# Kernel tuning notes

Hardware: AMD Instinct MI355X
Metric: run time of the kernel (lower is better)

Reference implementation:

```python
import jax, jax.numpy as jnp
import numpy as np

B, S, D_MODEL = 2, 2048, 2048
H, DS, DG, DV = 16, 64, 64, 128
ROPE_BASE = 10000.0
NEG_INF = -1e9


def _rope(x, base=ROPE_BASE):
    # x: [B, S, H, D] -> rotate-half RoPE over positions 0..S-1
    d = x.shape[-1]
    half = d // 2
    inv_freq = 1.0 / (base ** (jnp.arange(half, dtype=jnp.float32) / half))
    ang = jnp.arange(x.shape[1], dtype=jnp.float32)[:, None] * inv_freq  # [S, half]
    cos = jnp.cos(ang)[None, :, None, :]
    sin = jnp.sin(ang)[None, :, None, :]
    x1, x2 = x[..., :half], x[..., half:]
    return jnp.concatenate([x1 * cos - x2 * sin, x1 * sin + x2 * cos], axis=-1)


def setup_inputs() -> dict:
    key = jax.random.key(0)
    ks = jax.random.split(key, 8)
    s = lambda fan_in: 1.0 / np.sqrt(fan_in)
    return {
        "x": jax.random.normal(ks[0], (B, S, D_MODEL), dtype=jnp.float32),
        "wq_sem": jax.random.normal(ks[1], (D_MODEL, H * DS), dtype=jnp.float32) * s(D_MODEL),
        "wk_sem": jax.random.normal(ks[2], (D_MODEL, H * DS), dtype=jnp.float32) * s(D_MODEL),
        "wq_geo": jax.random.normal(ks[3], (D_MODEL, H * DG), dtype=jnp.float32) * s(D_MODEL),
        "wk_geo": jax.random.normal(ks[4], (D_MODEL, H * DG), dtype=jnp.float32) * s(D_MODEL),
        "wv": jax.random.normal(ks[5], (D_MODEL, H * DV), dtype=jnp.float32) * s(D_MODEL),
        "wo": jax.random.normal(ks[6], (H * DV, D_MODEL), dtype=jnp.float32) * s(H * DV),
        "gate_logit": jax.random.normal(ks[7], (H,), dtype=jnp.float32),
    }


def reference(x, wq_sem, wk_sem, wq_geo, wk_geo, wv, wo, gate_logit):
    b, sl, _ = x.shape
    # Projections -> [B, S, H, d]
    qs = (x @ wq_sem).reshape(b, sl, H, DS)
    ksem = (x @ wk_sem).reshape(b, sl, H, DS)
    qg = _rope((x @ wq_geo).reshape(b, sl, H, DG))
    kg = _rope((x @ wk_geo).reshape(b, sl, H, DG))
    v = (x @ wv).reshape(b, sl, H, DV)

    sem_scale = 1.0 / np.sqrt(DS)
    geo_scale = 1.0 / np.sqrt(DG)
    sem_scores = jnp.einsum("bqhd,bkhd->bhqk", qs, ksem) * sem_scale
    geo_scores = jnp.einsum("bqhd,bkhd->bhqk", qg, kg) * geo_scale

    # Learned per-head gate mixing semantic vs geometric paths
    g = jax.nn.sigmoid(gate_logit)[None, :, None, None]
    scores = g * sem_scores + (1.0 - g) * geo_scores

    causal = jnp.tril(jnp.ones((sl, sl), dtype=bool))
    scores = jnp.where(causal[None, None], scores, NEG_INF)
    attn = jax.nn.softmax(scores, axis=-1)

    out = jnp.einsum("bhqk,bkhd->bqhd", attn, v).reshape(b, sl, H * DV)
    return out @ wo
```

## Files before the change

### kernel.cpp

```cpp
#include <hip/hip_runtime.h>
#include <hip/hip_bf16.h>

typedef unsigned short u16;
typedef __attribute__((ext_vector_type(4))) float floatx4;
typedef __attribute__((ext_vector_type(8))) __bf16 bf16x8;

__device__ __forceinline__ u16 f2bf(float f) {
  unsigned int x = __builtin_bit_cast(unsigned int, f);
  unsigned int r = (x + 0x7fffu + ((x >> 16) & 1u)) >> 16;
  return (u16)r;
}
__device__ __forceinline__ float bf2f(u16 u) {
  unsigned int x = ((unsigned int)u) << 16;
  return __builtin_bit_cast(float, x);
}
__device__ __forceinline__ floatx4 mfma16(bf16x8 a, bf16x8 b, floatx4 c) {
  return __builtin_amdgcn_mfma_f32_16x16x32_bf16(a, b, c, 0, 0, 0);
}
__device__ __forceinline__ void gload16(const u16* g, u16* l) {
  __builtin_amdgcn_global_load_lds(
      (const __attribute__((address_space(1))) unsigned int*)g,
      (__attribute__((address_space(3))) unsigned int*)l, 16, 0, 0);
}
#define SCHEDB() __builtin_amdgcn_sched_barrier(0)
#define SBAR() __builtin_amdgcn_s_barrier()

#define BB 2
#define SS 2048
#define DM 2048
#define HH 16
#define PCOLS 6144

__global__ void convert_bf16_k(const float* __restrict__ src, u16* __restrict__ dst, size_t n) {
  size_t i = ((size_t)blockIdx.x * blockDim.x + threadIdx.x) * 4;
  if (i + 3 >= n) { for (size_t j = i; j < n; ++j) dst[j] = f2bf(src[j]); return; }
  float4 v = *(const float4*)&src[i];
  ushort4 o; o.x = f2bf(v.x); o.y = f2bf(v.y); o.z = f2bf(v.z); o.w = f2bf(v.w);
  *(ushort4*)&dst[i] = o;
}

__global__ void transpose_all_k(const float* w0, const float* w1, const float* w2,
                                const float* w3, const float* w4, const float* w5,
                                u16* __restrict__ WcatT, u16* __restrict__ WoT) {
  __shared__ float tile[32][33];
  const int z = blockIdx.z;
  const float* src; u16* dst; int cols;
  if (z == 0)      { src = w0; dst = WcatT;                        cols = 1024; }
  else if (z == 1) { src = w1; dst = WcatT + (size_t)1024 * 2048;  cols = 1024; }
  else if (z == 2) { src = w2; dst = WcatT + (size_t)2048 * 2048;  cols = 1024; }
  else if (z == 3) { src = w3; dst = WcatT + (size_t)3072 * 2048;  cols = 1024; }
  else if (z == 4) { src = w4; dst = WcatT + (size_t)4096 * 2048;  cols = 2048; }
  else             { src = w5; dst = WoT;                          cols = 2048; }
  int c0 = blockIdx.x * 32;
  if (c0 >= cols) return;
  int r0 = blockIdx.y * 32;
  int tx = threadIdx.x, ty = threadIdx.y;
#pragma unroll
  for (int i = 0; i < 4; ++i)
    tile[ty + i * 8][tx] = src[(size_t)(r0 + ty + i * 8) * cols + c0 + tx];
  __syncthreads();
#pragma unroll
  for (int i = 0; i < 4; ++i)
    dst[(size_t)(c0 + ty + i * 8) * 2048 + r0 + tx] = f2bf(tile[tx][ty + i * 8]);
}

__global__ void vtrans_k(const u16* __restrict__ P, u16* __restrict__ VtG) {
  __shared__ u16 t[32][33];
  int b = blockIdx.z;
  int c0 = blockIdx.x * 32;
  int s0 = blockIdx.y * 32;
  int tx = threadIdx.x, ty = threadIdx.y;
#pragma unroll
  for (int i = 0; i < 4; ++i)
    t[ty + i * 8][tx] = P[((size_t)b * SS + s0 + ty + i * 8) * PCOLS + 4096 + c0 + tx];
  __syncthreads();
#pragma unroll
  for (int i = 0; i < 4; ++i)
    VtG[((size_t)b * 2048 + c0 + ty + i * 8) * SS + s0 + tx] = t[tx][ty + i * 8];
}

__global__ void rope_table_k(float* __restrict__ cosT, float* __restrict__ sinT) {
  int idx = blockIdx.x * 256 + threadIdx.x;
  int s = idx >> 5, d = idx & 31;
  double inv = pow(10000.0, -(double)d / 32.0);
  double ang = (double)s * inv;
  cosT[idx] = (float)cos(ang);
  sinT[idx] = (float)sin(ang);
}

__global__ void rope_apply_k(u16* __restrict__ P, const float* __restrict__ cosT,
                             const float* __restrict__ sinT) {
  int idx = blockIdx.x * 256 + threadIdx.x;
  int d = idx & 31, h = (idx >> 5) & 15, reg = (idx >> 9) & 1, row = idx >> 10;
  int s = row & (SS - 1);
  size_t base = (size_t)row * PCOLS + (reg ? 3072 : 2048) + h * 64 + d;
  float x1 = bf2f(P[base]), x2 = bf2f(P[base + 32]);
  float c = cosT[s * 32 + d], sn = sinT[s * 32 + d];
  P[base] = f2bf(x1 * c - x2 * sn);
  P[base + 32] = f2bf(x1 * sn + x2 * c);
}

template <bool OUTF32>
__global__ __launch_bounds__(512, 2)
void gemm8_k(const u16* __restrict__ A, const u16* __restrict__ Bt,
             void* __restrict__ Cout, int M, int N, int K) {
  __shared__ alignas(16) u16 lds[49152];
  const int tid = threadIdx.x;
  const int wid = tid >> 6, lane = tid & 63;
  const int lr = lane & 15, lg = lane >> 4;
  const int wr = wid >> 2, wc = wid & 3;
  const int m0 = blockIdx.y * 128, n0 = blockIdx.x * 256;
  const int NT = K >> 6;
  const int NT4 = NT * 4;

  const int gA = ((lg ^ ((lr >> 1) & 3)) * 8);
  const int aoffL = lr * 32 + gA;

  const int srow = tid >> 2;
  const int sgl = (((tid & 3) ^ ((tid >> 3) & 3)) * 8);
  const u16* Asrc = A + (size_t)(m0 + srow) * K + sgl;
  const u16* Bsrc0 = Bt + (size_t)(n0 + srow) * K + sgl;
  const u16* Bsrc1 = Bsrc0 + (size_t)128 * K;
  const int wbase = wid * 512;

  floatx4 acc[4][4];
#pragma unroll
  for (int m = 0; m < 4; ++m)
#pragma unroll
    for (int n = 0; n < 4; ++n) acc[m][n] = (floatx4){0.f, 0.f, 0.f, 0.f};

  auto stgA = [&](int tile, int kh) {
    gload16(Asrc + tile * 64 + kh * 32,
            lds + ((tile & 1) * 2 + kh) * 4096 + wbase);
  };
  auto stgB = [&](int tile, int kh) {
    u16* d = lds + 16384 + ((tile & 1) * 2 + kh) * 8192 + wbase;
    const u16* s0 = Bsrc0 + tile * 64 + kh * 32;
    const u16* s1 = Bsrc1 + tile * 64 + kh * 32;
    gload16(s0, d);
    gload16(s1, d + 4096);
  };
  auto stage_slab = [&](int s) {
    if (s >= NT4) return;
    int tile = s >> 2, kind = s & 3;
    if (kind == 0) stgA(tile, 0);
    else if (kind == 1) stgB(tile, 0);
    else if (kind == 2) stgA(tile, 1);
    else stgB(tile, 1);
  };

  for (int s = 0; s < 7; ++s) stage_slab(s);
  asm volatile("s_waitcnt vmcnt(4)" ::: "memory");
  SCHEDB(); SBAR(); SCHEDB();

  bf16x8 af[4], bfv[2];

#pragma unroll 1
  for (int it = 0; it < (NT >> 1); ++it) {
    const int t = it * 2;
    const int sb = t * 4 + 6;
    const bool more = (t + 2 < NT);

#define PH(BUF, KK, NH, SL, DOVM)                                              \
    {                                                                          \
      const u16* Ab = lds + ((BUF) * 2 + (KK)) * 4096;                         \
      const u16* Bb = lds + 16384 + ((BUF) * 2 + (KK)) * 8192;                 \
      if ((NH) == 0) {                                                         \
        _Pragma("unroll") for (int m = 0; m < 4; ++m)                          \
          af[m] = *(const bf16x8*)&Ab[(wr * 64 + m * 16) * 32 + aoffL];        \
      }                                                                        \
      _Pragma("unroll") for (int j = 0; j < 2; ++j)                            \
        bfv[j] = *(const bf16x8*)&Bb[(wc * 64 + ((NH) * 2 + j) * 16) * 32 + aoffL]; \
      stage_slab(sb + (SL));                                                   \
      SCHEDB(); SBAR(); SCHEDB();                                              \
      __builtin_amdgcn_s_setprio(1);                                           \
      _Pragma("unroll") for (int m = 0; m < 4; ++m)                            \
        _Pragma("unroll") for (int j = 0; j < 2; ++j)                          \
          acc[m][(NH) * 2 + j] = mfma16(af[m], bfv[j], acc[m][(NH) * 2 + j]);  \
      __builtin_amdgcn_s_setprio(0);                                           \
      if (DOVM) {                                                              \
        if (more) asm volatile("s_waitcnt vmcnt(4)" ::: "memory");             \
        else      asm volatile("s_waitcnt vmcnt(0)" ::: "memory");             \
      }                                                                        \
      SCHEDB(); SBAR(); SCHEDB();                                              \
    }

    PH(0, 0, 0, 1, 0)
    PH(0, 0, 1, 2, 0)
    PH(0, 1, 0, 3, 0)
    PH(0, 1, 1, 4, 1)
    PH(1, 0, 0, 5, 0)
    PH(1, 0, 1, 6, 0)
    PH(1, 1, 0, 7, 0)
    PH(1, 1, 1, 8, 1)
#undef PH
  }

#pragma unroll
  for (int m = 0; m < 4; ++m) {
    int row0 = m0 + wr * 64 + m * 16 + lg * 4;
#pragma unroll
    for (int n = 0; n < 4; ++n) {
      int col = n0 + wc * 64 + n * 16 + lr;
#pragma unroll
      for (int r = 0; r < 4; ++r) {
        size_t off = (size_t)(row0 + r) * N + col;
        if (OUTF32) ((float*)Cout)[off] = acc[m][n][r];
        else        ((u16*)Cout)[off] = f2bf(acc[m][n][r]);
      }
    }
  }
}

__device__ __forceinline__ bf16x8 load_scaled(const u16* p, float s) {
  uint4 raw = *(const uint4*)p;
  const u16* ru = (const u16*)&raw;
  bf16x8 out;
#pragma unroll
  for (int j = 0; j < 8; ++j) out[j] = (__bf16)(bf2f(ru[j]) * s);
  return out;
}

__global__ __launch_bounds__(256, 3)
void attn_k(const u16* __restrict__ P, const u16* __restrict__ VtG,
            const float* __restrict__ gate, u16* __restrict__ AttO) {
  const int pairi = blockIdx.x >> 4;
  const int h = blockIdx.x & 15;
  const int b = blockIdx.y;
  const int tid = threadIdx.x, wid = tid >> 6, lane = tid & 63;
  const int lr = lane & 15, lg = lane >> 4;
  const size_t rowb = (size_t)b * SS;

  const float g = 1.f / (1.f + __expf(-gate[h]));
  const float ssc = g * 0.125f;
  const float gsc = (1.f - g) * 0.125f;

  __shared__ alignas(16) u16 Ks[64 * 64];
  __shared__ alignas(16) u16 Kg[64 * 64];
  __shared__ alignas(16) u16 Vt[128 * 64];
  __shared__ alignas(16) u16 Pw[4][16 * 64];

  const int strow = tid >> 3;
  const int stg = ((tid & 7) ^ (strow & 7)) * 8;
  const int swz = lr & 7;

  for (int half = 0; half < 2; ++half) {
    const int qb = half ? (31 - pairi) : pairi;
    const int q0 = qb * 64;

    const u16* qbase = P + (rowb + q0 + wid * 16 + lr) * PCOLS + h * 64;
    bf16x8 qs[2], qg[2];
#pragma unroll
    for (int kk = 0; kk < 2; ++kk) {
      qs[kk] = load_scaled(qbase + kk * 32 + lg * 8, ssc);
      qg[kk] = load_scaled(qbase + 2048 + kk * 32 + lg * 8, gsc);
    }

    float m_r = -1e30f, l_r = 0.f;
    floatx4 o[8];
#pragma unroll
    for (int n = 0; n < 8; ++n) o[n] = (floatx4){0.f, 0.f, 0.f, 0.f};

    const int nkv = q0 + 64;
    for (int kv0 = 0; kv0 < nkv; kv0 += 64) {
      __syncthreads();
      {
        const u16* ks = P + (rowb + kv0 + strow) * PCOLS + 1024 + h * 64 + stg;
        const u16* gs = P + (rowb + kv0 + strow) * PCOLS + 3072 + h * 64 + stg;
        gload16(ks, Ks + wid * 512);
        gload16(gs, Kg + wid * 512);
        gload16(ks + (size_t)32 * PCOLS, Ks + 2048 + wid * 512);
        gload16(gs + (size_t)32 * PCOLS, Kg + 2048 + wid * 512);
      }
      {
        const u16* vs = VtG + ((size_t)b * 2048 + h * 128 + strow) * SS + kv0 + stg;
#pragma unroll
        for (int c = 0; c < 4; ++c)
          gload16(vs + (size_t)(c * 32) * SS, Vt + c * 2048 + wid * 512);
      }
      __syncthreads();

      floatx4 sc[4];
#pragma unroll
      for (int s = 0; s < 4; ++s) sc[s] = (floatx4){0.f, 0.f, 0.f, 0.f};
#pragma unroll
      for (int kk = 0; kk < 2; ++kk) {
#pragma unroll
        for (int s = 0; s < 4; ++s) {
          bf16x8 kf = *(const bf16x8*)&Ks[(s * 16 + lr) * 64 + ((kk * 4 + lg) ^ swz) * 8];
          bf16x8 gf = *(const bf16x8*)&Kg[(s * 16 + lr) * 64 + ((kk * 4 + lg) ^ swz) * 8];
          sc[s] = mfma16(kf, qs[kk], sc[s]);
          sc[s] = mfma16(gf, qg[kk], sc[s]);
        }
      }

      const int qrow = q0 + wid * 16 + lr;
      const bool needmask = (kv0 + 63 > q0 + wid * 16);
      float vv[4][4];
      float vmax = -1e30f;
#pragma unroll
      for (int s = 0; s < 4; ++s)
#pragma unroll
        for (int r = 0; r < 4; ++r) {
          float val = sc[s][r];
          if (needmask) val = (kv0 + s * 16 + lg * 4 + r <= qrow) ? val : -1e30f;
          vv[s][r] = val;
          vmax = fmaxf(vmax, val);
        }
      vmax = fmaxf(vmax, __shfl_xor(vmax, 16));
      vmax = fmaxf(vmax, __shfl_xor(vmax, 32));
      float mnew = fmaxf(m_r, vmax);
      float corr = __expf(m_r - mnew);
      float psum = 0.f;
#pragma unroll
      for (int s = 0; s < 4; ++s)
#pragma unroll
        for (int r = 0; r < 4; ++r) {
          vv[s][r] = __expf(vv[s][r] - mnew);
          psum += vv[s][r];
        }
      psum += __shfl_xor(psum, 16);
      psum += __shfl_xor(psum, 32);
      l_r = l_r * corr + psum;
      m_r = mnew;

#pragma unroll
      for (int s = 0; s < 4; ++s)
#pragma unroll
        for (int t = 0; t < 2; ++t) {
          unsigned int w;
          asm("v_cvt_pk_bf16_f32 %0, %1, %2" : "=v"(w) : "v"(vv[s][2 * t]), "v"(vv[s][2 * t + 1]));
          int u16off = lr * 64 + ((s * 2 + (lg >> 1)) ^ swz) * 8 + (lg & 1) * 4 + t * 2;
          *(unsigned int*)&Pw[wid][u16off] = w;
        }

      float crr[4];
#pragma unroll
      for (int r = 0; r < 4; ++r) crr[r] = __shfl(corr, lg * 4 + r);
#pragma unroll
      for (int n = 0; n < 8; ++n)
#pragma unroll
        for (int r = 0; r < 4; ++r) o[n][r] *= crr[r];

      asm volatile("s_waitcnt lgkmcnt(0)" ::: "memory");
      SCHEDB();
      bf16x8 pa0 = *(const bf16x8*)&Pw[wid][lr * 64 + (lg ^ swz) * 8];
      bf16x8 pa1 = *(const bf16x8*)&Pw[wid][lr * 64 + ((4 + lg) ^ swz) * 8];
#pragma unroll
      for (int n = 0; n < 8; ++n) {
        bf16x8 vb0 = *(const bf16x8*)&Vt[(n * 16 + lr) * 64 + (lg ^ swz) * 8];
        bf16x8 vb1 = *(const bf16x8*)&Vt[(n * 16 + lr) * 64 + ((4 + lg) ^ swz) * 8];
        o[n] = mfma16(pa0, vb0, o[n]);
        o[n] = mfma16(pa1, vb1, o[n]);
      }
    }

    float linv = 1.f / l_r;
    float lnv[4];
#pragma unroll
    for (int r = 0; r < 4; ++r) lnv[r] = __shfl(linv, lg * 4 + r);
#pragma unroll
    for (int n = 0; n < 8; ++n)
#pragma unroll
      for (int r = 0; r < 4; ++r) {
        float val = o[n][r] * lnv[r];
        AttO[(rowb + q0 + wid * 16 + lg * 4 + r) * (size_t)(HH * 128) + h * 128 + n * 16 + lr] =
            f2bf(val);
      }
  }
}

extern "C" void kernel_launch(void* const* d_in, const int* in_sizes, int n_in,
                              void* d_out, int out_size, void* d_ws, size_t ws_size,
                              hipStream_t stream) {
  const float* x       = (const float*)d_in[0];
  const float* wq_sem  = (const float*)d_in[1];
  const float* wk_sem  = (const float*)d_in[2];
  const float* wq_geo  = (const float*)d_in[3];
  const float* wk_geo  = (const float*)d_in[4];
  const float* wv      = (const float*)d_in[5];
  const float* wo      = (const float*)d_in[6];
  const float* gate    = (const float*)d_in[7];

  char* ws = (char*)d_ws;
  u16* Xbf   = (u16*)(ws);
  u16* WcatT = (u16*)(ws + 16777216);
  u16* WoT   = (u16*)(ws + 16777216 + 25165824);
  u16* P     = (u16*)(ws + 16777216 + 25165824 + 8388608);
  float* cosT = (float*)(ws + 16777216 + 25165824 + 8388608 + 50331648);
  float* sinT = cosT + 2048 * 32;
  u16* AttO = Xbf;
  u16* VtG  = WcatT;

  dim3 tb(32, 8);
  convert_bf16_k<<<8192, 256, 0, stream>>>(x, Xbf, (size_t)4096 * 2048);
  transpose_all_k<<<dim3(64, 64, 6), tb, 0, stream>>>(wq_sem, wk_sem, wq_geo, wk_geo,
                                                      wv, wo, WcatT, WoT);
  rope_table_k<<<256, 256, 0, stream>>>(cosT, sinT);

  gemm8_k<false><<<dim3(24, 32), 512, 0, stream>>>(Xbf, WcatT, P, 4096, 6144, 2048);
  rope_apply_k<<<16384, 256, 0, stream>>>(P, cosT, sinT);
  vtrans_k<<<dim3(64, 64, 2), tb, 0, stream>>>(P, VtG);
  attn_k<<<dim3(256, 2), 256, 0, stream>>>(P, VtG, gate, AttO);
  gemm8_k<true><<<dim3(8, 32), 512, 0, stream>>>(AttO, WoT, d_out, 4096, 2048, 2048);
}
```

Before: 272.2 us.

## Replace 8-wave GEMM with 4-wave kernel using larger per-wave tiles

The 512-thread GEMM (128x256 tile, 2x4 wave grid) is replaced by a 256-thread, one-block-per-SM kernel in which each wave computes all 128 rows against its own NFB*16 columns. The QKV projection now uses 128x384 tiles (512 blocks instead of 768) and the output projection uses 128x256 tiles. Larger per-wave register tiles raise MFMA work per LDS fragment load. The cost is more accumulator registers, fewer resident waves to hide latency, and changed vmcnt wait thresholds.

```diff
diff --git a/kernel.cpp b/kernel.cpp
--- a/kernel.cpp
+++ b/kernel.cpp
@@ -100,48 +100,46 @@
   P[base + 32] = f2bf(x1 * sn + x2 * c);
 }
 
-template <bool OUTF32>
-__global__ __launch_bounds__(512, 2)
-void gemm8_k(const u16* __restrict__ A, const u16* __restrict__ Bt,
+template <int NFB, bool OUTF32>
+__global__ __launch_bounds__(256, 1)
+void gemm4_k(const u16* __restrict__ A, const u16* __restrict__ Bt,
              void* __restrict__ Cout, int M, int N, int K) {
-  __shared__ alignas(16) u16 lds[49152];
+  constexpr int BH = NFB / 2;
+  __shared__ alignas(16) u16 lds[16384 + NFB * 8192];
   const int tid = threadIdx.x;
   const int wid = tid >> 6, lane = tid & 63;
   const int lr = lane & 15, lg = lane >> 4;
-  const int wr = wid >> 2, wc = wid & 3;
-  const int m0 = blockIdx.y * 128, n0 = blockIdx.x * 256;
+  const int m0 = blockIdx.y * 128, n0 = blockIdx.x * (NFB * 64);
   const int NT = K >> 6;
-  const int NT4 = NT * 4;
-
-  const int gA = ((lg ^ ((lr >> 1) & 3)) * 8);
-  const int aoffL = lr * 32 + gA;
-
-  const int srow = tid >> 2;
-  const int sgl = (((tid & 3) ^ ((tid >> 3) & 3)) * 8);
+  const int NSLAB = NT * 4;
+
+  const int aoff = lr * 32 + ((lg ^ ((lr >> 1) & 3)) * 8);
+
+  const int srow = wid * 16 + (lane >> 2);
+  const int sgl = (((lane & 3) ^ ((lane >> 3) & 3)) * 8);
   const u16* Asrc = A + (size_t)(m0 + srow) * K + sgl;
-  const u16* Bsrc0 = Bt + (size_t)(n0 + srow) * K + sgl;
-  const u16* Bsrc1 = Bsrc0 + (size_t)128 * K;
-  const int wbase = wid * 512;
-
-  floatx4 acc[4][4];
-#pragma unroll
-  for (int m = 0; m < 4; ++m)
-#pragma unroll
-    for (int n = 0; n < 4; ++n) acc[m][n] = (floatx4){0.f, 0.f, 0.f, 0.f};
+  const u16* Bsrc = Bt + (size_t)(n0 + srow) * K + sgl;
+
+  floatx4 acc[8][NFB];
+#pragma unroll
+  for (int m = 0; m < 8; ++m)
+#pragma unroll
+    for (int n = 0; n < NFB; ++n) acc[m][n] = (floatx4){0.f, 0.f, 0.f, 0.f};
 
   auto stgA = [&](int tile, int kh) {
-    gload16(Asrc + tile * 64 + kh * 32,
-            lds + ((tile & 1) * 2 + kh) * 4096 + wbase);
+    u16* d = lds + ((tile & 1) * 2 + kh) * 4096 + wid * 512;
+    const u16* s = Asrc + tile * 64 + kh * 32;
+#pragma unroll
+    for (int c = 0; c < 2; ++c) gload16(s + (size_t)(c * 64) * K, d + c * 2048);
   };
   auto stgB = [&](int tile, int kh) {
-    u16* d = lds + 16384 + ((tile & 1) * 2 + kh) * 8192 + wbase;
-    const u16* s0 = Bsrc0 + tile * 64 + kh * 32;
-    const u16* s1 = Bsrc1 + tile * 64 + kh * 32;
-    gload16(s0, d);
-    gload16(s1, d + 4096);
+    u16* d = lds + 16384 + ((tile & 1) * 2 + kh) * (NFB * 2048) + wid * 512;
+    const u16* s = Bsrc + tile * 64 + kh * 32;
+#pragma unroll
+    for (int c = 0; c < NFB; ++c) gload16(s + (size_t)(c * 64) * K, d + c * 2048);
   };
   auto stage_slab = [&](int s) {
-    if (s >= NT4) return;
+    if (s >= NSLAB) return;
     int tile = s >> 2, kind = s & 3;
     if (kind == 0) stgA(tile, 0);
     else if (kind == 1) stgB(tile, 0);
@@ -150,10 +148,11 @@
   };
 
   for (int s = 0; s < 7; ++s) stage_slab(s);
-  asm volatile("s_waitcnt vmcnt(4)" ::: "memory");
+  if constexpr (NFB == 6) asm volatile("s_waitcnt vmcnt(10)" ::: "memory");
+  else                    asm volatile("s_waitcnt vmcnt(8)" ::: "memory");
   SCHEDB(); SBAR(); SCHEDB();
 
-  bf16x8 af[4], bfv[2];
+  bf16x8 af[8], bfv[BH];
 
 #pragma unroll 1
   for (int it = 0; it < (NT >> 1); ++it) {
@@ -161,28 +160,32 @@
     const int sb = t * 4 + 6;
     const bool more = (t + 2 < NT);
 
-#define PH(BUF, KK, NH, SL, DOVM)                                              \
-    {                                                                          \
-      const u16* Ab = lds + ((BUF) * 2 + (KK)) * 4096;                         \
-      const u16* Bb = lds + 16384 + ((BUF) * 2 + (KK)) * 8192;                 \
-      if ((NH) == 0) {                                                         \
-        _Pragma("unroll") for (int m = 0; m < 4; ++m)                          \
-          af[m] = *(const bf16x8*)&Ab[(wr * 64 + m * 16) * 32 + aoffL];        \
-      }                                                                        \
-      _Pragma("unroll") for (int j = 0; j < 2; ++j)                            \
-        bfv[j] = *(const bf16x8*)&Bb[(wc * 64 + ((NH) * 2 + j) * 16) * 32 + aoffL]; \
-      stage_slab(sb + (SL));                                                   \
-      SCHEDB(); SBAR(); SCHEDB();                                              \
-      __builtin_amdgcn_s_setprio(1);                                           \
-      _Pragma("unroll") for (int m = 0; m < 4; ++m)                            \
-        _Pragma("unroll") for (int j = 0; j < 2; ++j)                          \
-          acc[m][(NH) * 2 + j] = mfma16(af[m], bfv[j], acc[m][(NH) * 2 + j]);  \
-      __builtin_amdgcn_s_setprio(0);                                           \
-      if (DOVM) {                                                              \
-        if (more) asm volatile("s_waitcnt vmcnt(4)" ::: "memory");             \
-        else      asm volatile("s_waitcnt vmcnt(0)" ::: "memory");             \
-      }                                                                        \
-      SCHEDB(); SBAR(); SCHEDB();                                              \
+#define PH(BUF, KK, NH, SL, DOVM)                                               \
+    {                                                                           \
+      const u16* Ab = lds + ((BUF) * 2 + (KK)) * 4096;                          \
+      const u16* Bb = lds + 16384 + ((BUF) * 2 + (KK)) * (NFB * 2048);          \
+      if ((NH) == 0) {                                                          \
+        _Pragma("unroll") for (int m = 0; m < 8; ++m)                           \
+          af[m] = *(const bf16x8*)&Ab[(m * 16) * 32 + aoff];                    \
+      }                                                                         \
+      _Pragma("unroll") for (int j = 0; j < BH; ++j)                            \
+        bfv[j] = *(const bf16x8*)&Bb[(wid * NFB * 16 + ((NH) * BH + j) * 16) * 32 + aoff]; \
+      stage_slab(sb + (SL));                                                    \
+      SCHEDB(); SBAR(); SCHEDB();                                               \
+      __builtin_amdgcn_s_setprio(1);                                            \
+      _Pragma("unroll") for (int m = 0; m < 8; ++m)                             \
+        _Pragma("unroll") for (int j = 0; j < BH; ++j)                          \
+          acc[m][(NH) * BH + j] = mfma16(af[m], bfv[j], acc[m][(NH) * BH + j]); \
+      __builtin_amdgcn_s_setprio(0);                                            \
+      if (DOVM) {                                                               \
+        if (more) {                                                             \
+          if constexpr (NFB == 6) asm volatile("s_waitcnt vmcnt(10)" ::: "memory"); \
+          else                    asm volatile("s_waitcnt vmcnt(8)" ::: "memory");  \
+        } else {                                                                \
+          asm volatile("s_waitcnt vmcnt(0)" ::: "memory");                      \
+        }                                                                       \
+      }                                                                         \
+      SCHEDB(); SBAR(); SCHEDB();                                               \
     }
 
     PH(0, 0, 0, 1, 0)
@@ -197,11 +200,11 @@
   }
 
 #pragma unroll
-  for (int m = 0; m < 4; ++m) {
-    int row0 = m0 + wr * 64 + m * 16 + lg * 4;
-#pragma unroll
-    for (int n = 0; n < 4; ++n) {
-      int col = n0 + wc * 64 + n * 16 + lr;
+  for (int m = 0; m < 8; ++m) {
+    int row0 = m0 + m * 16 + lg * 4;
+#pragma unroll
+    for (int n = 0; n < NFB; ++n) {
+      int col = n0 + wid * NFB * 16 + n * 16 + lr;
 #pragma unroll
       for (int r = 0; r < 4; ++r) {
         size_t off = (size_t)(row0 + r) * N + col;
@@ -398,9 +401,9 @@
                                                       wv, wo, WcatT, WoT);
   rope_table_k<<<256, 256, 0, stream>>>(cosT, sinT);
 
-  gemm8_k<false><<<dim3(24, 32), 512, 0, stream>>>(Xbf, WcatT, P, 4096, 6144, 2048);
+  gemm4_k<6, false><<<dim3(16, 32), 256, 0, stream>>>(Xbf, WcatT, P, 4096, 6144, 2048);
   rope_apply_k<<<16384, 256, 0, stream>>>(P, cosT, sinT);
   vtrans_k<<<dim3(64, 64, 2), tb, 0, stream>>>(P, VtG);
   attn_k<<<dim3(256, 2), 256, 0, stream>>>(P, VtG, gate, AttO);
-  gemm8_k<true><<<dim3(8, 32), 512, 0, stream>>>(AttO, WoT, d_out, 4096, 2048, 2048);
-}
+  gemm4_k<4, true><<<dim3(8, 32), 256, 0, stream>>>(AttO, WoT, d_out, 4096, 2048, 2048);
+}
```

After: 266.0 us. 1.02x faster.

## Restructure GEMM pipeline into coarser half-tile phases with XCD-aware block swizzle

Applied to the files above, without the earlier changes.

Rewrites the GEMM main loop from eight fine-grained phases, each issuing one A or B slab, into four phases. Each phase loads all 16 MFMA operand fragments and stages a combined A+B half-tile. It also remaps the block index with a modulo-8 swizzle so neighbouring tiles land on the same chiplet for L2 reuse, and lowers the occupancy hint to one block per CU. The aim is fewer barriers and better cache locality, at the cost of a deeper vmcnt wait window and possibly lower occupancy or register pressure changes.

```diff
diff --git a/kernel.cpp b/kernel.cpp
--- a/kernel.cpp
+++ b/kernel.cpp
@@ -101,27 +101,27 @@
 }
 
 template <bool OUTF32>
-__global__ __launch_bounds__(512, 2)
-void gemm8_k(const u16* __restrict__ A, const u16* __restrict__ Bt,
+__global__ __launch_bounds__(512, 1)
+void gemm2_k(const u16* __restrict__ A, const u16* __restrict__ Bt,
              void* __restrict__ Cout, int M, int N, int K) {
   __shared__ alignas(16) u16 lds[49152];
   const int tid = threadIdx.x;
   const int wid = tid >> 6, lane = tid & 63;
   const int lr = lane & 15, lg = lane >> 4;
   const int wr = wid >> 2, wc = wid & 3;
-  const int m0 = blockIdx.y * 128, n0 = blockIdx.x * 256;
+  const int nwgx = gridDim.x;
+  const int nwg = nwgx * gridDim.y;
+  const int lin = blockIdx.y * nwgx + blockIdx.x;
+  const int swz = (lin & 7) * (nwg >> 3) + (lin >> 3);
+  const int m0 = (swz / nwgx) * 128, n0 = (swz % nwgx) * 256;
   const int NT = K >> 6;
-  const int NT4 = NT * 4;
-
-  const int gA = ((lg ^ ((lr >> 1) & 3)) * 8);
-  const int aoffL = lr * 32 + gA;
+
+  const int aoff = lr * 32 + ((lg ^ ((lr >> 1) & 3)) * 8);
 
   const int srow = tid >> 2;
   const int sgl = (((tid & 3) ^ ((tid >> 3) & 3)) * 8);
   const u16* Asrc = A + (size_t)(m0 + srow) * K + sgl;
-  const u16* Bsrc0 = Bt + (size_t)(n0 + srow) * K + sgl;
-  const u16* Bsrc1 = Bsrc0 + (size_t)128 * K;
-  const int wbase = wid * 512;
+  const u16* Bsrc = Bt + (size_t)(n0 + srow) * K + sgl;
 
   floatx4 acc[4][4];
 #pragma unroll
@@ -129,70 +129,50 @@
 #pragma unroll
     for (int n = 0; n < 4; ++n) acc[m][n] = (floatx4){0.f, 0.f, 0.f, 0.f};
 
-  auto stgA = [&](int tile, int kh) {
-    gload16(Asrc + tile * 64 + kh * 32,
-            lds + ((tile & 1) * 2 + kh) * 4096 + wbase);
+  auto stage_half = [&](int tile, int kh) {
+    if (tile >= NT) return;
+    const int rb = (tile & 1) * 2 + kh;
+    gload16(Asrc + tile * 64 + kh * 32, lds + rb * 4096 + wid * 512);
+    u16* db = lds + 16384 + rb * 8192 + wid * 512;
+    const u16* sb = Bsrc + tile * 64 + kh * 32;
+    gload16(sb, db);
+    gload16(sb + (size_t)128 * K, db + 4096);
   };
-  auto stgB = [&](int tile, int kh) {
-    u16* d = lds + 16384 + ((tile & 1) * 2 + kh) * 8192 + wbase;
-    const u16* s0 = Bsrc0 + tile * 64 + kh * 32;
-    const u16* s1 = Bsrc1 + tile * 64 + kh * 32;
-    gload16(s0, d);
-    gload16(s1, d + 4096);
-  };
-  auto stage_slab = [&](int s) {
-    if (s >= NT4) return;
-    int tile = s >> 2, kind = s & 3;
-    if (kind == 0) stgA(tile, 0);
-    else if (kind == 1) stgB(tile, 0);
-    else if (kind == 2) stgA(tile, 1);
-    else stgB(tile, 1);
-  };
-
-  for (int s = 0; s < 7; ++s) stage_slab(s);
-  asm volatile("s_waitcnt vmcnt(4)" ::: "memory");
+
+  stage_half(0, 0); stage_half(0, 1); stage_half(1, 0);
+  asm volatile("s_waitcnt vmcnt(3)" ::: "memory");
   SCHEDB(); SBAR(); SCHEDB();
 
-  bf16x8 af[4], bfv[2];
+  bf16x8 af[4], bfv[4];
 
 #pragma unroll 1
   for (int it = 0; it < (NT >> 1); ++it) {
     const int t = it * 2;
-    const int sb = t * 4 + 6;
-    const bool more = (t + 2 < NT);
-
-#define PH(BUF, KK, NH, SL, DOVM)                                              \
-    {                                                                          \
-      const u16* Ab = lds + ((BUF) * 2 + (KK)) * 4096;                         \
-      const u16* Bb = lds + 16384 + ((BUF) * 2 + (KK)) * 8192;                 \
-      if ((NH) == 0) {                                                         \
-        _Pragma("unroll") for (int m = 0; m < 4; ++m)                          \
-          af[m] = *(const bf16x8*)&Ab[(wr * 64 + m * 16) * 32 + aoffL];        \
-      }                                                                        \
-      _Pragma("unroll") for (int j = 0; j < 2; ++j)                            \
-        bfv[j] = *(const bf16x8*)&Bb[(wc * 64 + ((NH) * 2 + j) * 16) * 32 + aoffL]; \
-      stage_slab(sb + (SL));                                                   \
-      SCHEDB(); SBAR(); SCHEDB();                                              \
-      __builtin_amdgcn_s_setprio(1);                                           \
-      _Pragma("unroll") for (int m = 0; m < 4; ++m)                            \
-        _Pragma("unroll") for (int j = 0; j < 2; ++j)                          \
-          acc[m][(NH) * 2 + j] = mfma16(af[m], bfv[j], acc[m][(NH) * 2 + j]);  \
-      __builtin_amdgcn_s_setprio(0);                                           \
-      if (DOVM) {                                                              \
-        if (more) asm volatile("s_waitcnt vmcnt(4)" ::: "memory");             \
-        else      asm volatile("s_waitcnt vmcnt(0)" ::: "memory");             \
-      }                                                                        \
-      SCHEDB(); SBAR(); SCHEDB();                                              \
+
+#define PH(BUF, KK, STILE, SKH, MORE)                                       \
+    {                                                                       \
+      const u16* Ab = lds + ((BUF) * 2 + (KK)) * 4096;                      \
+      const u16* Bb = lds + 16384 + ((BUF) * 2 + (KK)) * 8192;              \
+      _Pragma("unroll") for (int m = 0; m < 4; ++m)                         \
+        af[m] = *(const bf16x8*)&Ab[(wr * 64 + m * 16) * 32 + aoff];        \
+      _Pragma("unroll") for (int n = 0; n < 4; ++n)                         \
+        bfv[n] = *(const bf16x8*)&Bb[(wc * 64 + n * 16) * 32 + aoff];       \
+      stage_half((STILE), (SKH));                                           \
+      SCHEDB(); SBAR(); SCHEDB();                                           \
+      __builtin_amdgcn_s_setprio(1);                                        \
+      _Pragma("unroll") for (int m = 0; m < 4; ++m)                         \
+        _Pragma("unroll") for (int n = 0; n < 4; ++n)                       \
+          acc[m][n] = mfma16(af[m], bfv[n], acc[m][n]);                     \
+      __builtin_amdgcn_s_setprio(0);                                        \
+      if (MORE) asm volatile("s_waitcnt vmcnt(6)" ::: "memory");            \
+      else      asm volatile("s_waitcnt vmcnt(0)" ::: "memory");            \
+      SCHEDB(); SBAR(); SCHEDB();                                           \
     }
 
-    PH(0, 0, 0, 1, 0)
-    PH(0, 0, 1, 2, 0)
-    PH(0, 1, 0, 3, 0)
-    PH(0, 1, 1, 4, 1)
-    PH(1, 0, 0, 5, 0)
-    PH(1, 0, 1, 6, 0)
-    PH(1, 1, 0, 7, 0)
-    PH(1, 1, 1, 8, 1)
+    PH(0, 0, t + 1, 1, (t + 2 < NT))
+    PH(0, 1, t + 2, 0, (t + 2 < NT))
+    PH(1, 0, t + 2, 1, (t + 3 < NT))
+    PH(1, 1, t + 3, 0, (t + 3 < NT))
 #undef PH
   }
 
@@ -398,9 +378,9 @@
                                                       wv, wo, WcatT, WoT);
   rope_table_k<<<256, 256, 0, stream>>>(cosT, sinT);
 
-  gemm8_k<false><<<dim3(24, 32), 512, 0, stream>>>(Xbf, WcatT, P, 4096, 6144, 2048);
+  gemm2_k<false><<<dim3(24, 32), 512, 0, stream>>>(Xbf, WcatT, P, 4096, 6144, 2048);
   rope_apply_k<<<16384, 256, 0, stream>>>(P, cosT, sinT);
   vtrans_k<<<dim3(64, 64, 2), tb, 0, stream>>>(P, VtG);
   attn_k<<<dim3(256, 2), 256, 0, stream>>>(P, VtG, gate, AttO);
-  gemm8_k<true><<<dim3(8, 32), 512, 0, stream>>>(AttO, WoT, d_out, 4096, 2048, 2048);
-}
+  gemm2_k<true><<<dim3(8, 32), 512, 0, stream>>>(AttO, WoT, d_out, 4096, 2048, 2048);
+}
```

Measured after the change: 275.7 us. No clear change (+1.3%).
